# Optimization experiments

Measured on AMD Instinct MI355X. Metric: run time of the kernel, lower is better.

## Reference

```python
import jax, jax.numpy as jnp
import numpy as np

B, N, S = 4, 16384, 16384
C1, C2 = 256, 256
D_MODEL, NHEAD, OUT_DIM = 256, 8, 256
HEAD_DIM = D_MODEL // NHEAD
EPS_ATTN = 1e-6


def _layernorm(x, g, b, eps=1e-5):
    mu = jnp.mean(x, axis=-1, keepdims=True)
    var = jnp.mean(jnp.square(x - mu), axis=-1, keepdims=True)
    return (x - mu) * jax.lax.rsqrt(var + eps) * g + b


def setup_inputs() -> dict:
    key = jax.random.key(0)
    ks = jax.random.split(key, 20)
    def w(k, shape, fan_in):
        return jax.random.normal(k, shape, jnp.float32) * (1.0 / np.sqrt(fan_in))
    return {
        "feat1": jax.random.normal(ks[0], (B, C1, N), jnp.float32),
        "xyz1": jax.random.normal(ks[1], (B, N, 3), jnp.float32),
        "feat2": jax.random.normal(ks[2], (B, C2, S), jnp.float32),
        "xyz2": jax.random.normal(ks[3], (B, S, 3), jnp.float32),
        # pos_mlp2: Linear(3, d_model) -> ReLU -> Linear(d_model, feat2_dim)
        "pos_w1": w(ks[4], (D_MODEL, 3), 3),
        "pos_b1": jnp.zeros((D_MODEL,), jnp.float32),
        "pos_w2": w(ks[5], (C2, D_MODEL), D_MODEL),
        "pos_b2": jnp.zeros((C2,), jnp.float32),
        "q_w": w(ks[6], (D_MODEL, C1), C1),
        "k_w": w(ks[7], (D_MODEL, C2), C2),
        "v_w": w(ks[8], (D_MODEL, C2), C2),
        "merge_w": w(ks[9], (D_MODEL, D_MODEL), D_MODEL),
        # mlp: Linear(C1 + d_model, 2*d_model) -> ReLU -> Linear(2*d_model, out_dim)
        "mlp_w1": w(ks[10], (2 * D_MODEL, C1 + D_MODEL), C1 + D_MODEL),
        "mlp_w2": w(ks[11], (OUT_DIM, 2 * D_MODEL), 2 * D_MODEL),
        "ln1_g": jnp.ones((D_MODEL,), jnp.float32),
        "ln1_b": jnp.zeros((D_MODEL,), jnp.float32),
        "ln2_g": jnp.ones((OUT_DIM,), jnp.float32),
        "ln2_b": jnp.zeros((OUT_DIM,), jnp.float32),
    }


def reference(feat1, xyz1, feat2, xyz2, pos_w1, pos_b1, pos_w2, pos_b2,
              q_w, k_w, v_w, merge_w, mlp_w1, mlp_w2,
              ln1_g, ln1_b, ln2_g, ln2_b):
    bs = feat1.shape[0]
    f1 = jnp.transpose(feat1, (0, 2, 1))  # [B, N, C1]
    f2 = jnp.transpose(feat2, (0, 2, 1))  # [B, S, C2]
    # positional MLP on xyz2 added to feat2
    pos = jax.nn.relu(xyz2 @ pos_w1.T + pos_b1) @ pos_w2.T + pos_b2
    f2p = f2 + pos
    q = (f1 @ q_w.T).reshape(bs, -1, NHEAD, HEAD_DIM)   # [B, N, H, D]
    k = (f2 @ k_w.T).reshape(bs, -1, NHEAD, HEAD_DIM)   # [B, S, H, D]
    v = (f2p @ v_w.T).reshape(bs, -1, NHEAD, HEAD_DIM)  # [B, S, H, D]
    # Linear attention (elu feature map)
    Q = jax.nn.elu(q) + 1.0
    K = jax.nn.elu(k) + 1.0
    v_len = v.shape[1]
    V = v / v_len
    KV = jnp.einsum('nshd,nshv->nhdv', K, V)                 # [B, H, D, D]
    Z = 1.0 / (jnp.einsum('nlhd,nhd->nlh', Q, K.sum(axis=1)) + EPS_ATTN)
    msg = jnp.einsum('nlhd,nhdv,nlh->nlhv', Q, KV, Z) * v_len  # [B, N, H, D]
    msg = msg.reshape(bs, -1, NHEAD * HEAD_DIM) @ merge_w.T
    msg = _layernorm(msg, ln1_g, ln1_b)
    msg = jnp.concatenate([f1, msg], axis=2)
    msg = jax.nn.relu(msg @ mlp_w1.T) @ mlp_w2.T
    msg = _layernorm(msg, ln2_g, ln2_b)
    return jnp.transpose(msg, (0, 2, 1))  # [B, out_dim, N]
```

## Files before the change

kernel.cpp:

```cpp
#include <hip/hip_runtime.h>


typedef float f32x4 __attribute__((ext_vector_type(4)));
typedef __bf16 bf16x8 __attribute__((ext_vector_type(8)));
typedef __bf16 bf16x4 __attribute__((ext_vector_type(4)));

#define MFMA16(a, b, c) __builtin_amdgcn_mfma_f32_16x16x32_bf16((a), (b), (c), 0, 0, 0)

__device__ __forceinline__ void gll16(const __bf16* g, __bf16* l) {
    __builtin_amdgcn_global_load_lds(
        (const __attribute__((address_space(1))) void*)g,
        (__attribute__((address_space(3))) void*)l, 16, 0, 0);
}

__global__ __launch_bounds__(256) void prep_weights_kernel(
    const float* __restrict__ s0, const float* __restrict__ s1,
    const float* __restrict__ s2, const float* __restrict__ s3,
    const float* __restrict__ s4, const float* __restrict__ s5,
    const float* __restrict__ s6,
    __bf16* __restrict__ d0, __bf16* __restrict__ d1, __bf16* __restrict__ d2,
    __bf16* __restrict__ d3, __bf16* __restrict__ d4, __bf16* __restrict__ d5,
    __bf16* __restrict__ d6, float* __restrict__ zbase)
{
    int idx = blockIdx.x * 256 + threadIdx.x;
    if (idx < 327680) {
        int seg = idx >> 16, off = idx & 65535;
        const float* s = (seg == 0) ? s0 : (seg == 1) ? s1 : (seg == 2) ? s2 : (seg == 3) ? s3 : s4;
        __bf16* d = (seg == 0) ? d0 : (seg == 1) ? d1 : (seg == 2) ? d2 : (seg == 3) ? d3 : d4;
        d[off] = (__bf16)s[off];
    } else if (idx < 589824) {
        int off = idx - 327680; d5[off] = (__bf16)s5[off];
    } else if (idx < 720896) {
        int off = idx - 589824; d6[off] = (__bf16)s6[off];
    } else if (idx < 754688) {
        zbase[idx - 720896] = 0.f;
    }
}

__global__ __launch_bounds__(256) void pos_hidden_kernel(
    const float* __restrict__ xyz2, const float* __restrict__ pw1,
    const float* __restrict__ pb1, __bf16* __restrict__ Hid)
{
    const int tid = threadIdx.x;
    size_t tok = (size_t)blockIdx.x * 8 + (tid >> 5);
    int c0 = (tid & 31) * 8;
    const float* xz = xyz2 + tok * 3;
    float x = xz[0], y = xz[1], z = xz[2];
    bf16x8 o;
    #pragma unroll
    for (int j = 0; j < 8; ++j) {
        const float* wr = pw1 + (size_t)(c0 + j) * 3;
        float h = fmaf(x, wr[0], fmaf(y, wr[1], fmaf(z, wr[2], pb1[c0 + j])));
        o[j] = (__bf16)fmaxf(h, 0.f);
    }
    *(bf16x8*)(Hid + tok * 256 + c0) = o;
}

__global__ __launch_bounds__(256) void transpose_cast_kernel(
    const float* __restrict__ In, __bf16* __restrict__ Outb)
{
    const int tid = threadIdx.x;
    const int t0 = blockIdx.x * 64, c0 = blockIdx.y * 64;
    const size_t b = blockIdx.z;
    __shared__ __bf16 tile[64 * 72];
    #pragma unroll
    for (int i = 0; i < 4; ++i) {
        int c = i * 16 + (tid >> 4);
        int t4 = (tid & 15) * 4;
        float4 v = *(const float4*)(In + (b * 256 + c0 + c) * 16384 + t0 + t4);
        tile[(t4 + 0) * 72 + c] = (__bf16)v.x;
        tile[(t4 + 1) * 72 + c] = (__bf16)v.y;
        tile[(t4 + 2) * 72 + c] = (__bf16)v.z;
        tile[(t4 + 3) * 72 + c] = (__bf16)v.w;
    }
    __syncthreads();
    #pragma unroll
    for (int i = 0; i < 2; ++i) {
        int chunk = tid + i * 256;
        int tr = chunk >> 3, c8 = (chunk & 7) * 8;
        bf16x8 v = *(const bf16x8*)(tile + tr * 72 + c8);
        *(bf16x8*)(Outb + (b * 16384 + t0 + tr) * 256 + c0 + c8) = v;
    }
}

enum { EPI_STORE = 0, EPI_ELU = 1, EPI_ADDB = 2, EPI_RELU = 3, EPI_ELU_KSUM = 4 };

template <int EPI, bool SPLIT>
__global__ __launch_bounds__(256, 2) void gemm_tok(
    const __bf16* __restrict__ Wg,
    const __bf16* __restrict__ A0,
    const __bf16* __restrict__ A1,
    __bf16* __restrict__ Outg,
    const float* __restrict__ bias,
    const __bf16* __restrict__ addg,
    float* __restrict__ KSg,
    int K, int Cout)
{
    const int tid = threadIdx.x, w = tid >> 6, l = tid & 63, lm = l & 15;
    const int gm0 = blockIdx.x * 128, gn0 = blockIdx.y * 128;
    const size_t b = blockIdx.z;
    const __bf16* A0b = A0 + b * 16384 * (size_t)256;
    const __bf16* A1b = SPLIT ? (A1 + b * 16384 * (size_t)256) : nullptr;
    __bf16* Outb = Outg + b * 16384 * (size_t)Cout;
    const __bf16* addb = (EPI == EPI_ADDB) ? (addg + b * 16384 * (size_t)256) : nullptr;

    __shared__ __bf16 Alds[128 * 32];
    __shared__ __bf16 Wlds[128 * 32];
    __shared__ float kred[16 * 64];

    f32x4 acc[4][4];
    #pragma unroll
    for (int i = 0; i < 4; ++i)
        #pragma unroll
        for (int j = 0; j < 4; ++j) acc[i][j] = (f32x4){0.f, 0.f, 0.f, 0.f};

    const int wm = (w >> 1) * 64, wn = (w & 1) * 64;
    const int srow = tid >> 2, scol = (tid & 3) * 8;
    const int koff = (l >> 4) * 8;
    const int wbase = w * 512;

    for (int ks = 0; ks < K; ks += 32) {
        const __bf16* As = A0b; int kk = ks;
        if (SPLIT && ks >= 256) { As = A1b; kk = ks - 256; }
        __syncthreads();
        gll16(As + (size_t)(gm0 + srow) * 256 + kk + scol,      Alds + wbase);
        gll16(As + (size_t)(gm0 + 64 + srow) * 256 + kk + scol, Alds + 2048 + wbase);
        gll16(Wg + (size_t)(gn0 + srow) * K + ks + scol,        Wlds + wbase);
        gll16(Wg + (size_t)(gn0 + 64 + srow) * K + ks + scol,   Wlds + 2048 + wbase);
        __syncthreads();
        bf16x8 af[4], wf[4];
        #pragma unroll
        for (int mf = 0; mf < 4; ++mf)
            af[mf] = *(const bf16x8*)(Alds + (wm + mf * 16 + lm) * 32 + koff);
        #pragma unroll
        for (int nf = 0; nf < 4; ++nf)
            wf[nf] = *(const bf16x8*)(Wlds + (wn + nf * 16 + lm) * 32 + koff);
        #pragma unroll
        for (int mf = 0; mf < 4; ++mf)
            #pragma unroll
            for (int nf = 0; nf < 4; ++nf)
                acc[mf][nf] = MFMA16(af[mf], wf[nf], acc[mf][nf]);
    }

    const int r0 = (l >> 4) * 4;
    float kpart[4] = {0.f, 0.f, 0.f, 0.f};
    #pragma unroll
    for (int mf = 0; mf < 4; ++mf) {
        #pragma unroll
        for (int nf = 0; nf < 4; ++nf) {
            int tok = gm0 + wm + mf * 16 + r0;
            int ch  = gn0 + wn + nf * 16 + lm;
            #pragma unroll
            for (int r = 0; r < 4; ++r) {
                float v = acc[mf][nf][r];
                if (EPI == EPI_ELU || EPI == EPI_ELU_KSUM)
                    v = (v > 0.f) ? (v + 1.f) : __expf(v);
                if (EPI == EPI_RELU) v = fmaxf(v, 0.f);
                if (EPI == EPI_ADDB) v = v + bias[ch] + (float)addb[(size_t)(tok + r) * 256 + ch];
                if (EPI == EPI_ELU_KSUM) kpart[nf] += v;
                Outb[(size_t)(tok + r) * Cout + ch] = (__bf16)v;
            }
        }
    }
    if (EPI == EPI_ELU_KSUM) {
        #pragma unroll
        for (int nf = 0; nf < 4; ++nf)
            kred[(w * 4 + (l >> 4)) * 64 + nf * 16 + lm] = kpart[nf];
        __syncthreads();
        if (tid < 128) {
            int c = tid;
            int wsel = (c >= 64) ? 1 : 0;
            float s = 0.f;
            #pragma unroll
            for (int q = 0; q < 4; ++q)
                s += kred[((wsel * 4) + q) * 64 + (c & 63)]
                   + kred[(((wsel + 2) * 4) + q) * 64 + (c & 63)];
            atomicAdd(&KSg[b * 256 + gn0 + c], s);
        }
    }
}

__global__ __launch_bounds__(256) void kv_kernel(
    const __bf16* __restrict__ Kb, const __bf16* __restrict__ Vb,
    float* __restrict__ KVg)
{
    const int tid = threadIdx.x, w = tid >> 6, l = tid & 63, lm = l & 15;
    const int sc = blockIdx.x, h = blockIdx.y, b = blockIdx.z;
    __shared__ __bf16 kT[32 * 264];
    __shared__ __bf16 vT[32 * 264];
    __shared__ float red[4 * 32 * 32];

    f32x4 acc[2][2];
    #pragma unroll
    for (int i = 0; i < 2; ++i)
        #pragma unroll
        for (int j = 0; j < 2; ++j) acc[i][j] = (f32x4){0.f, 0.f, 0.f, 0.f};

    const int koff = (l >> 4) * 8, r0 = (l >> 4) * 4;
    for (int sub = 0; sub < 4; ++sub) {
        int s0 = sc * 1024 + sub * 256;
        __syncthreads();
        for (int pass = 0; pass < 8; ++pass) {
            int sl = pass * 32 + (tid >> 3);
            int c4 = (tid & 7) * 4;
            bf16x4 kv4 = *(const bf16x4*)(Kb + ((size_t)b * 16384 + s0 + sl) * 256 + h * 32 + c4);
            bf16x4 vv4 = *(const bf16x4*)(Vb + ((size_t)b * 16384 + s0 + sl) * 256 + h * 32 + c4);
            #pragma unroll
            for (int i = 0; i < 4; ++i) {
                kT[(c4 + i) * 264 + sl] = kv4[i];
                vT[(c4 + i) * 264 + sl] = vv4[i];
            }
        }
        __syncthreads();
        #pragma unroll
        for (int kq = 0; kq < 2; ++kq) {
            int sb = w * 64 + kq * 32;
            bf16x8 af[2], bfr[2];
            #pragma unroll
            for (int mf = 0; mf < 2; ++mf)
                af[mf] = *(const bf16x8*)(kT + (mf * 16 + lm) * 264 + sb + koff);
            #pragma unroll
            for (int nf = 0; nf < 2; ++nf)
                bfr[nf] = *(const bf16x8*)(vT + (nf * 16 + lm) * 264 + sb + koff);
            #pragma unroll
            for (int mf = 0; mf < 2; ++mf)
                #pragma unroll
                for (int nf = 0; nf < 2; ++nf)
                    acc[mf][nf] = MFMA16(af[mf], bfr[nf], acc[mf][nf]);
        }
    }
    #pragma unroll
    for (int mf = 0; mf < 2; ++mf)
        #pragma unroll
        for (int nf = 0; nf < 2; ++nf)
            #pragma unroll
            for (int r = 0; r < 4; ++r) {
                int d = mf * 16 + r0 + r, e = nf * 16 + lm;
                red[w * 1024 + d * 32 + e] = acc[mf][nf][r];
            }
    __syncthreads();
    #pragma unroll
    for (int i = 0; i < 4; ++i) {
        int idx = tid + i * 256;
        float s = red[idx] + red[1024 + idx] + red[2048 + idx] + red[3072 + idx];
        atomicAdd(&KVg[((size_t)(b * 8 + h)) * 1024 + idx], s);
    }
}

__global__ __launch_bounds__(256) void attn_apply(
    const __bf16* __restrict__ Qb, const float* __restrict__ KVg,
    const float* __restrict__ KSg, __bf16* __restrict__ Msg)
{
    const int tid = threadIdx.x, w = tid >> 6, l = tid & 63, lm = l & 15;
    const int tok0 = blockIdx.x * 64;
    const size_t b = blockIdx.y;
    __shared__ __bf16 kvT[8 * 32 * 40];
    __shared__ float ks_lds[256], z_lds[64 * 8];

    const float* KVb = KVg + b * 8192;
    #pragma unroll
    for (int i = 0; i < 32; ++i) {
        int idx = tid + i * 256;
        int h = idx >> 10, d = (idx >> 5) & 31, e = idx & 31;
        kvT[(h * 32 + e) * 40 + d] = (__bf16)KVb[idx];
    }
    ks_lds[tid] = KSg[b * 256 + tid];
    __syncthreads();

    const __bf16* Qbase = Qb + (b * 16384 + tok0) * (size_t)256;
    #pragma unroll
    for (int i = 0; i < 2; ++i) {
        int p = tid + i * 256;
        int tok = p >> 3, h = p & 7;
        const __bf16* qr = Qbase + (size_t)tok * 256 + h * 32;
        float s = 0.f;
        #pragma unroll
        for (int j = 0; j < 4; ++j) {
            bf16x8 q8 = *(const bf16x8*)(qr + j * 8);
            #pragma unroll
            for (int t = 0; t < 8; ++t) s += (float)q8[t] * ks_lds[h * 32 + j * 8 + t];
        }
        z_lds[tok * 8 + h] = 1.f / (s + 1e-6f);
    }
    __syncthreads();

    const int koff = (l >> 4) * 8, r0 = (l >> 4) * 4;
    const f32x4 zero4 = (f32x4){0.f, 0.f, 0.f, 0.f};
    #pragma unroll
    for (int h = 0; h < 8; ++h) {
        bf16x8 af = *(const bf16x8*)(Qbase + (size_t)(w * 16 + lm) * 256 + h * 32 + koff);
        #pragma unroll
        for (int nf = 0; nf < 2; ++nf) {
            bf16x8 bv = *(const bf16x8*)(kvT + (h * 32 + nf * 16 + lm) * 40 + koff);
            f32x4 m = MFMA16(af, bv, zero4);
            #pragma unroll
            for (int r = 0; r < 4; ++r) {
                int tok = w * 16 + r0 + r;
                Msg[(b * 16384 + tok0 + tok) * (size_t)256 + h * 32 + nf * 16 + lm] =
                    (__bf16)(m[r] * z_lds[tok * 8 + h]);
            }
        }
    }
}

template <bool TRANS>
__global__ __launch_bounds__(256, 2) void gemm_ln(
    const __bf16* __restrict__ Ag,
    const __bf16* __restrict__ Wg,
    const float* __restrict__ gv, const float* __restrict__ bv,
    __bf16* __restrict__ OutB,
    float* __restrict__ OutF,
    int K)
{
    const int tid = threadIdx.x, w = tid >> 6, l = tid & 63, lm = l & 15;
    const int tok0 = blockIdx.x * 128;
    const size_t b = blockIdx.y;
    const size_t trow = b * 16384 + tok0;

    __shared__ __bf16 Alds[128 * 32];
    __shared__ __bf16 Wlds[256 * 32];
    __shared__ float red1[4 * 128], red2[4 * 128], mu_lds[128], rs_lds[128];
    __shared__ float g_lds[256], b_lds[256];
    g_lds[tid] = gv[tid];
    b_lds[tid] = bv[tid];

    f32x4 acc[8][4];
    #pragma unroll
    for (int i = 0; i < 8; ++i)
        #pragma unroll
        for (int j = 0; j < 4; ++j) acc[i][j] = (f32x4){0.f, 0.f, 0.f, 0.f};

    const int srow = tid >> 2, scol = (tid & 3) * 8;
    const int koff = (l >> 4) * 8, wn = w * 64, wbase = w * 512;

    for (int ks = 0; ks < K; ks += 32) {
        __syncthreads();
        gll16(Ag + (trow + srow) * K + ks + scol,        Alds + wbase);
        gll16(Ag + (trow + 64 + srow) * K + ks + scol,   Alds + 2048 + wbase);
        #pragma unroll
        for (int c = 0; c < 4; ++c)
            gll16(Wg + (size_t)(c * 64 + srow) * K + ks + scol, Wlds + c * 2048 + wbase);
        __syncthreads();
        bf16x8 af[8], wf[4];
        #pragma unroll
        for (int mf = 0; mf < 8; ++mf)
            af[mf] = *(const bf16x8*)(Alds + (mf * 16 + lm) * 32 + koff);
        #pragma unroll
        for (int nf = 0; nf < 4; ++nf)
            wf[nf] = *(const bf16x8*)(Wlds + (wn + nf * 16 + lm) * 32 + koff);
        #pragma unroll
        for (int mf = 0; mf < 8; ++mf)
            #pragma unroll
            for (int nf = 0; nf < 4; ++nf)
                acc[mf][nf] = MFMA16(af[mf], wf[nf], acc[mf][nf]);
    }

    const int r0 = (l >> 4) * 4;
    #pragma unroll
    for (int mf = 0; mf < 8; ++mf) {
        #pragma unroll
        for (int r = 0; r < 4; ++r) {
            float s1 = 0.f, s2 = 0.f;
            #pragma unroll
            for (int nf = 0; nf < 4; ++nf) { float v = acc[mf][nf][r]; s1 += v; s2 += v * v; }
            #pragma unroll
            for (int m = 1; m < 16; m <<= 1) { s1 += __shfl_xor(s1, m, 64); s2 += __shfl_xor(s2, m, 64); }
            if (lm == 0) {
                red1[w * 128 + mf * 16 + r0 + r] = s1;
                red2[w * 128 + mf * 16 + r0 + r] = s2;
            }
        }
    }
    __syncthreads();
    if (tid < 128) {
        float s1 = red1[tid] + red1[128 + tid] + red1[256 + tid] + red1[384 + tid];
        float s2 = red2[tid] + red2[128 + tid] + red2[256 + tid] + red2[384 + tid];
        float mu = s1 * (1.f / 256.f);
        mu_lds[tid] = mu;
        rs_lds[tid] = rsqrtf(s2 * (1.f / 256.f) - mu * mu + 1e-5f);
    }
    __syncthreads();

    if (TRANS) {
        #pragma unroll
        for (int mf = 0; mf < 8; ++mf) {
            #pragma unroll
            for (int nf = 0; nf < 4; ++nf) {
                int ch = wn + nf * 16 + lm;
                int tl = mf * 16 + r0;
                float4 v;
                v.x = (acc[mf][nf][0] - mu_lds[tl + 0]) * rs_lds[tl + 0] * g_lds[ch] + b_lds[ch];
                v.y = (acc[mf][nf][1] - mu_lds[tl + 1]) * rs_lds[tl + 1] * g_lds[ch] + b_lds[ch];
                v.z = (acc[mf][nf][2] - mu_lds[tl + 2]) * rs_lds[tl + 2] * g_lds[ch] + b_lds[ch];
                v.w = (acc[mf][nf][3] - mu_lds[tl + 3]) * rs_lds[tl + 3] * g_lds[ch] + b_lds[ch];
                *(float4*)(OutF + (b * 256 + ch) * (size_t)16384 + tok0 + tl) = v;
            }
        }
    } else {
        #pragma unroll
        for (int mf = 0; mf < 8; ++mf) {
            #pragma unroll
            for (int nf = 0; nf < 4; ++nf) {
                int ch = wn + nf * 16 + lm;
                #pragma unroll
                for (int r = 0; r < 4; ++r) {
                    int tl = mf * 16 + r0 + r;
                    float y = (acc[mf][nf][r] - mu_lds[tl]) * rs_lds[tl] * g_lds[ch] + b_lds[ch];
                    OutB[(trow + tl) * (size_t)256 + ch] = (__bf16)y;
                }
            }
        }
    }
}

extern "C" void kernel_launch(void* const* d_in, const int* in_sizes, int n_in,
                              void* d_out, int out_size, void* d_ws, size_t ws_size,
                              hipStream_t stream) {
    const float* feat1   = (const float*)d_in[0];
    const float* feat2   = (const float*)d_in[2];
    const float* xyz2    = (const float*)d_in[3];
    const float* pos_w1  = (const float*)d_in[4];
    const float* pos_b1  = (const float*)d_in[5];
    const float* pos_w2  = (const float*)d_in[6];
    const float* pos_b2  = (const float*)d_in[7];
    const float* q_w     = (const float*)d_in[8];
    const float* k_w     = (const float*)d_in[9];
    const float* v_w     = (const float*)d_in[10];
    const float* merge_w = (const float*)d_in[11];
    const float* mlp_w1  = (const float*)d_in[12];
    const float* mlp_w2  = (const float*)d_in[13];
    const float* ln1_g   = (const float*)d_in[14];
    const float* ln1_b   = (const float*)d_in[15];
    const float* ln2_g   = (const float*)d_in[16];
    const float* ln2_b   = (const float*)d_in[17];
    float* outp = (float*)d_out;

    char* ws = (char*)d_ws;
    size_t off = 0;
    auto alloc = [&](size_t bytes) { char* p = ws + off; off += (bytes + 255) & ~(size_t)255; return p; };
    const size_t ACT = (size_t)4 * 16384 * 256 * 2;
    __bf16* WQ  = (__bf16*)alloc(65536 * 2);
    __bf16* WK  = (__bf16*)alloc(65536 * 2);
    __bf16* WV  = (__bf16*)alloc(65536 * 2);
    __bf16* WM  = (__bf16*)alloc(65536 * 2);
    __bf16* WP2 = (__bf16*)alloc(65536 * 2);
    __bf16* W1  = (__bf16*)alloc(262144 * 2);
    __bf16* W2  = (__bf16*)alloc(131072 * 2);
    float*  KV  = (float*)alloc(4 * 8 * 32 * 32 * 4);
    float*  KS  = (float*)alloc(4 * 256 * 4);
    __bf16* F1T = (__bf16*)alloc(ACT);
    __bf16* HID = (__bf16*)alloc(ACT);
    __bf16* F2T = (__bf16*)alloc(ACT);
    __bf16* F2P = (__bf16*)alloc(ACT);
    __bf16* KB  = (__bf16*)alloc(ACT);
    __bf16* VB  = (__bf16*)alloc(ACT);
    __bf16* QB  = (__bf16*)alloc(ACT);
    __bf16* H1     = HID;
    __bf16* MSGRAW = F2T;
    __bf16* MSG1   = F2P;
    if (ws_size < off) return;

    prep_weights_kernel<<<2948, 256, 0, stream>>>(q_w, k_w, v_w, merge_w, pos_w2,
                                                  mlp_w1, mlp_w2,
                                                  WQ, WK, WV, WM, WP2, W1, W2, KV);
    pos_hidden_kernel<<<8192, 256, 0, stream>>>(xyz2, pos_w1, pos_b1, HID);
    transpose_cast_kernel<<<dim3(256, 4, 4), 256, 0, stream>>>(feat1, F1T);
    transpose_cast_kernel<<<dim3(256, 4, 4), 256, 0, stream>>>(feat2, F2T);
    gemm_tok<EPI_ADDB, false><<<dim3(128, 2, 4), 256, 0, stream>>>(WP2, HID, nullptr, F2P, pos_b2, F2T, nullptr, 256, 256);
    gemm_tok<EPI_ELU_KSUM, false><<<dim3(128, 2, 4), 256, 0, stream>>>(WK, F2T, nullptr, KB, nullptr, nullptr, KS, 256, 256);
    gemm_tok<EPI_STORE, false><<<dim3(128, 2, 4), 256, 0, stream>>>(WV, F2P, nullptr, VB, nullptr, nullptr, nullptr, 256, 256);
    gemm_tok<EPI_ELU, false><<<dim3(128, 2, 4), 256, 0, stream>>>(WQ, F1T, nullptr, QB, nullptr, nullptr, nullptr, 256, 256);
    kv_kernel<<<dim3(16, 8, 4), 256, 0, stream>>>(KB, VB, KV);
    attn_apply<<<dim3(256, 4), 256, 0, stream>>>(QB, KV, KS, MSGRAW);
    gemm_ln<false><<<dim3(128, 4), 256, 0, stream>>>(MSGRAW, WM, ln1_g, ln1_b, MSG1, nullptr, 256);
    gemm_tok<EPI_RELU, true><<<dim3(128, 4, 4), 256, 0, stream>>>(W1, F1T, MSG1, H1, nullptr, nullptr, nullptr, 512, 512);
    gemm_ln<true><<<dim3(128, 4), 256, 0, stream>>>(H1, W2, ln2_g, ln2_b, nullptr, outp, 512);
    (void)in_sizes; (void)n_in; (void)out_size;
}
```

Baseline: 453.8 us.

## Double-buffer GEMM LDS tiles, prefetch KV loads, stage transposed LN output

Adds double-buffered LDS staging to gemm_tok and gemm_ln, so the next K-slice is issued via global_load_lds before computing on the current one, with one barrier per iteration instead of two. kv_kernel now prefetches the next sub-chunk of K/V into registers while MFMAs run on the current chunk. The transposed LayerNorm output is staged through LDS per 16-channel group, so each store writes full 512-byte rows instead of scattered 16-byte float4s. gemm_tok's launch bound rises to 4 blocks per CU, which caps registers and may cause spills. The larger LDS footprint may lower occupancy for gemm_ln.

```diff
diff --git a/kernel.cpp b/kernel.cpp
--- a/kernel.cpp
+++ b/kernel.cpp
@@ -86,7 +86,7 @@
 enum { EPI_STORE = 0, EPI_ELU = 1, EPI_ADDB = 2, EPI_RELU = 3, EPI_ELU_KSUM = 4 };
 
 template <int EPI, bool SPLIT>
-__global__ __launch_bounds__(256, 2) void gemm_tok(
+__global__ __launch_bounds__(256, 4) void gemm_tok(
     const __bf16* __restrict__ Wg,
     const __bf16* __restrict__ A0,
     const __bf16* __restrict__ A1,
@@ -104,8 +104,8 @@
     __bf16* Outb = Outg + b * 16384 * (size_t)Cout;
     const __bf16* addb = (EPI == EPI_ADDB) ? (addg + b * 16384 * (size_t)256) : nullptr;
 
-    __shared__ __bf16 Alds[128 * 32];
-    __shared__ __bf16 Wlds[128 * 32];
+    __shared__ __bf16 Alds[2][128 * 32];
+    __shared__ __bf16 Wlds[2][128 * 32];
     __shared__ float kred[16 * 64];
 
     f32x4 acc[4][4];
@@ -119,27 +119,34 @@
     const int koff = (l >> 4) * 8;
     const int wbase = w * 512;
 
-    for (int ks = 0; ks < K; ks += 32) {
+    auto stage = [&](int buf, int ks) {
         const __bf16* As = A0b; int kk = ks;
         if (SPLIT && ks >= 256) { As = A1b; kk = ks - 256; }
-        __syncthreads();
-        gll16(As + (size_t)(gm0 + srow) * 256 + kk + scol,      Alds + wbase);
-        gll16(As + (size_t)(gm0 + 64 + srow) * 256 + kk + scol, Alds + 2048 + wbase);
-        gll16(Wg + (size_t)(gn0 + srow) * K + ks + scol,        Wlds + wbase);
-        gll16(Wg + (size_t)(gn0 + 64 + srow) * K + ks + scol,   Wlds + 2048 + wbase);
-        __syncthreads();
+        gll16(As + (size_t)(gm0 + srow) * 256 + kk + scol,      &Alds[buf][wbase]);
+        gll16(As + (size_t)(gm0 + 64 + srow) * 256 + kk + scol, &Alds[buf][2048 + wbase]);
+        gll16(Wg + (size_t)(gn0 + srow) * K + ks + scol,        &Wlds[buf][wbase]);
+        gll16(Wg + (size_t)(gn0 + 64 + srow) * K + ks + scol,   &Wlds[buf][2048 + wbase]);
+    };
+
+    stage(0, 0);
+    __syncthreads();
+    int cur = 0;
+    for (int ks = 0; ks < K; ks += 32) {
+        if (ks + 32 < K) stage(cur ^ 1, ks + 32);
         bf16x8 af[4], wf[4];
         #pragma unroll
         for (int mf = 0; mf < 4; ++mf)
-            af[mf] = *(const bf16x8*)(Alds + (wm + mf * 16 + lm) * 32 + koff);
+            af[mf] = *(const bf16x8*)&Alds[cur][(wm + mf * 16 + lm) * 32 + koff];
         #pragma unroll
         for (int nf = 0; nf < 4; ++nf)
-            wf[nf] = *(const bf16x8*)(Wlds + (wn + nf * 16 + lm) * 32 + koff);
+            wf[nf] = *(const bf16x8*)&Wlds[cur][(wn + nf * 16 + lm) * 32 + koff];
         #pragma unroll
         for (int mf = 0; mf < 4; ++mf)
             #pragma unroll
             for (int nf = 0; nf < 4; ++nf)
                 acc[mf][nf] = MFMA16(af[mf], wf[nf], acc[mf][nf]);
+        __syncthreads();
+        cur ^= 1;
     }
 
     const int r0 = (l >> 4) * 4;
@@ -197,21 +204,33 @@
         for (int j = 0; j < 2; ++j) acc[i][j] = (f32x4){0.f, 0.f, 0.f, 0.f};
 
     const int koff = (l >> 4) * 8, r0 = (l >> 4) * 4;
-    for (int sub = 0; sub < 4; ++sub) {
+    const size_t rowbase = (size_t)b * 16384;
+    bf16x4 kreg[8], vreg[8];
+    auto loadsub = [&](int sub) {
         int s0 = sc * 1024 + sub * 256;
-        __syncthreads();
+        #pragma unroll
         for (int pass = 0; pass < 8; ++pass) {
             int sl = pass * 32 + (tid >> 3);
             int c4 = (tid & 7) * 4;
-            bf16x4 kv4 = *(const bf16x4*)(Kb + ((size_t)b * 16384 + s0 + sl) * 256 + h * 32 + c4);
-            bf16x4 vv4 = *(const bf16x4*)(Vb + ((size_t)b * 16384 + s0 + sl) * 256 + h * 32 + c4);
+            kreg[pass] = *(const bf16x4*)(Kb + (rowbase + s0 + sl) * 256 + h * 32 + c4);
+            vreg[pass] = *(const bf16x4*)(Vb + (rowbase + s0 + sl) * 256 + h * 32 + c4);
+        }
+    };
+    loadsub(0);
+    for (int sub = 0; sub < 4; ++sub) {
+        __syncthreads();
+        #pragma unroll
+        for (int pass = 0; pass < 8; ++pass) {
+            int sl = pass * 32 + (tid >> 3);
+            int c4 = (tid & 7) * 4;
             #pragma unroll
             for (int i = 0; i < 4; ++i) {
-                kT[(c4 + i) * 264 + sl] = kv4[i];
-                vT[(c4 + i) * 264 + sl] = vv4[i];
+                kT[(c4 + i) * 264 + sl] = kreg[pass][i];
+                vT[(c4 + i) * 264 + sl] = vreg[pass][i];
             }
         }
         __syncthreads();
+        if (sub < 3) loadsub(sub + 1);
         #pragma unroll
         for (int kq = 0; kq < 2; ++kq) {
             int sb = w * 64 + kq * 32;
@@ -317,9 +336,10 @@
     const size_t b = blockIdx.y;
     const size_t trow = b * 16384 + tok0;
 
-    __shared__ __bf16 Alds[128 * 32];
-    __shared__ __bf16 Wlds[256 * 32];
-    __shared__ float red1[4 * 128], red2[4 * 128], mu_lds[128], rs_lds[128];
+    __shared__ __align__(16) char smem[49152];
+    __bf16* AldsB = (__bf16*)smem;
+    __bf16* WldsB = (__bf16*)(smem + 16384);
+    __shared__ float red1[512], red2[512], mu_lds[128], rs_lds[128];
     __shared__ float g_lds[256], b_lds[256];
     g_lds[tid] = gv[tid];
     b_lds[tid] = bv[tid];
@@ -333,26 +353,34 @@
     const int srow = tid >> 2, scol = (tid & 3) * 8;
     const int koff = (l >> 4) * 8, wn = w * 64, wbase = w * 512;
 
+    auto stage = [&](int buf, int ks) {
+        gll16(Ag + (trow + srow) * K + ks + scol,      AldsB + buf * 4096 + wbase);
+        gll16(Ag + (trow + 64 + srow) * K + ks + scol, AldsB + buf * 4096 + 2048 + wbase);
+        #pragma unroll
+        for (int c = 0; c < 4; ++c)
+            gll16(Wg + (size_t)(c * 64 + srow) * K + ks + scol,
+                  WldsB + buf * 8192 + c * 2048 + wbase);
+    };
+
+    stage(0, 0);
+    __syncthreads();
+    int cur = 0;
     for (int ks = 0; ks < K; ks += 32) {
-        __syncthreads();
-        gll16(Ag + (trow + srow) * K + ks + scol,        Alds + wbase);
-        gll16(Ag + (trow + 64 + srow) * K + ks + scol,   Alds + 2048 + wbase);
-        #pragma unroll
-        for (int c = 0; c < 4; ++c)
-            gll16(Wg + (size_t)(c * 64 + srow) * K + ks + scol, Wlds + c * 2048 + wbase);
-        __syncthreads();
+        if (ks + 32 < K) stage(cur ^ 1, ks + 32);
         bf16x8 af[8], wf[4];
         #pragma unroll
         for (int mf = 0; mf < 8; ++mf)
-            af[mf] = *(const bf16x8*)(Alds + (mf * 16 + lm) * 32 + koff);
+            af[mf] = *(const bf16x8*)(AldsB + cur * 4096 + (mf * 16 + lm) * 32 + koff);
         #pragma unroll
         for (int nf = 0; nf < 4; ++nf)
-            wf[nf] = *(const bf16x8*)(Wlds + (wn + nf * 16 + lm) * 32 + koff);
+            wf[nf] = *(const bf16x8*)(WldsB + cur * 8192 + (wn + nf * 16 + lm) * 32 + koff);
         #pragma unroll
         for (int mf = 0; mf < 8; ++mf)
             #pragma unroll
             for (int nf = 0; nf < 4; ++nf)
                 acc[mf][nf] = MFMA16(af[mf], wf[nf], acc[mf][nf]);
+        __syncthreads();
+        cur ^= 1;
     }
 
     const int r0 = (l >> 4) * 4;
@@ -382,18 +410,27 @@
     __syncthreads();
 
     if (TRANS) {
-        #pragma unroll
-        for (int mf = 0; mf < 8; ++mf) {
-            #pragma unroll
-            for (int nf = 0; nf < 4; ++nf) {
-                int ch = wn + nf * 16 + lm;
+        float* wb = (float*)smem + w * 2112;
+        #pragma unroll
+        for (int nf = 0; nf < 4; ++nf) {
+            __syncthreads();
+            float gg = g_lds[wn + nf * 16 + lm], bb = b_lds[wn + nf * 16 + lm];
+            #pragma unroll
+            for (int mf = 0; mf < 8; ++mf) {
                 int tl = mf * 16 + r0;
-                float4 v;
-                v.x = (acc[mf][nf][0] - mu_lds[tl + 0]) * rs_lds[tl + 0] * g_lds[ch] + b_lds[ch];
-                v.y = (acc[mf][nf][1] - mu_lds[tl + 1]) * rs_lds[tl + 1] * g_lds[ch] + b_lds[ch];
-                v.z = (acc[mf][nf][2] - mu_lds[tl + 2]) * rs_lds[tl + 2] * g_lds[ch] + b_lds[ch];
-                v.w = (acc[mf][nf][3] - mu_lds[tl + 3]) * rs_lds[tl + 3] * g_lds[ch] + b_lds[ch];
-                *(float4*)(OutF + (b * 256 + ch) * (size_t)16384 + tok0 + tl) = v;
+                f32x4 v;
+                #pragma unroll
+                for (int r = 0; r < 4; ++r)
+                    v[r] = (acc[mf][nf][r] - mu_lds[tl + r]) * rs_lds[tl + r] * gg + bb;
+                *(f32x4*)(wb + lm * 132 + tl) = v;
+            }
+            __syncthreads();
+            #pragma unroll
+            for (int t = 0; t < 8; ++t) {
+                int row = t * 2 + (l >> 5);
+                int col = (l & 31) * 4;
+                f32x4 v = *(const f32x4*)(wb + row * 132 + col);
+                *(f32x4*)(OutF + (b * 256 + wn + nf * 16 + row) * (size_t)16384 + tok0 + col) = v;
             }
         }
     } else {
```

New measurement: 454.2 us. About the same (+0.1%).
